# Performance work log

Hardware: AMD Instinct MI355X
Metric: run time of the kernel (lower is better)

The kernel has to match this reference:

```python
import jax, jax.numpy as jnp
import numpy as np

N = 20000      # nodes
E = 200000     # edges
F_IN = 512     # num_features
H = 1024       # hidden (hard-coded in module)
OUT = 128      # output_size


def setup_inputs() -> dict:
    key = jax.random.key(0)
    ks = jax.random.split(key, 12)
    x = jax.random.normal(ks[0], (N, F_IN), jnp.float32)
    edge_index = jax.random.randint(ks[1], (2, E), 0, N, dtype=jnp.int32)
    edge_weight = jax.random.uniform(ks[2], (E,), jnp.float32)
    # GCNConv weights (glorot-ish) and biases
    w1 = jax.random.normal(ks[3], (F_IN, H), jnp.float32) / np.sqrt(F_IN)
    b1 = jnp.zeros((H,), jnp.float32)
    w2 = jax.random.normal(ks[4], (H, OUT), jnp.float32) / np.sqrt(H)
    b2 = jnp.zeros((OUT,), jnp.float32)
    # residual Linear layers
    rw1 = jax.random.normal(ks[5], (F_IN, H), jnp.float32) / np.sqrt(F_IN)
    rb1 = jax.random.normal(ks[6], (H,), jnp.float32) * 0.01
    rw2 = jax.random.normal(ks[7], (H, OUT), jnp.float32) / np.sqrt(H)
    rb2 = jax.random.normal(ks[8], (OUT,), jnp.float32) * 0.01
    return {"x": x, "w1": w1, "b1": b1, "w2": w2, "b2": b2,
            "rw1": rw1, "rb1": rb1, "rw2": rw2, "rb2": rb2,
            "edge_weight": edge_weight, "edge_index": edge_index}


def gcn_conv(x, W, b, edge_index, edge_weight, n):
    """PyG GCNConv: linear transform, add self-loops (weight 1), sym-normalized scatter-add."""
    xw = x @ W                                             # [n, d_out]
    loop = jnp.arange(n, dtype=edge_index.dtype)
    row = jnp.concatenate([edge_index[0], loop])           # sources (x_j)
    col = jnp.concatenate([edge_index[1], loop])           # targets (aggregate here)
    ew = jnp.concatenate([edge_weight, jnp.ones((n,), xw.dtype)])
    deg = jax.ops.segment_sum(ew, col, num_segments=n)     # weighted in-degree
    dis = jnp.where(deg > 0, jax.lax.rsqrt(jnp.where(deg > 0, deg, 1.0)), 0.0)
    norm = dis[row] * ew * dis[col]                        # [E+n]
    msg = xw[row] * norm[:, None]                          # gather + scale
    out = jax.ops.segment_sum(msg, col, num_segments=n)    # scatter-add
    return out + b


def reference(x, w1, b1, w2, b2, rw1, rb1, rw2, rb2, edge_weight, edge_index):
    n = x.shape[0]
    h = jax.nn.relu(gcn_conv(x, w1, b1, edge_index, edge_weight, n) + (x @ rw1 + rb1))
    # F.dropout(training=False) is identity in eval mode
    out = gcn_conv(h, w2, b2, edge_index, edge_weight, n) + (h @ rw2 + rb2)
    return out
```

## Files before the change

kernel.cpp:

```cpp
#include <hip/hip_runtime.h>
#include <hip/hip_bf16.h>

#define NN 20000
#define EE 200000
#define FIN 512
#define HID 1024
#define OUTF 128
#define MPAD 20096

typedef unsigned short ush;
typedef __attribute__((ext_vector_type(8))) short bf16x8;
typedef __attribute__((ext_vector_type(4))) float f32x4;

__device__ __forceinline__ ush f2bf_rne(float f) {
    union { float f; unsigned u; } a; a.f = f;
    unsigned u = a.u;
    return (ush)((u + 0x7fffu + ((u >> 16) & 1u)) >> 16);
}
__device__ __forceinline__ float bf2f(ush h) {
    union { float f; unsigned u; } a; a.u = ((unsigned)h) << 16;
    return a.f;
}
__device__ __forceinline__ void split_bf(float v, ush& hi, ush& lo) {
    hi = f2bf_rne(v);
    lo = f2bf_rne(v - bf2f(hi));
}

__device__ __forceinline__ void gl16(const void* g, void* l) {
    __builtin_amdgcn_global_load_lds(
        (const __attribute__((address_space(1))) unsigned*)g,
        (__attribute__((address_space(3))) unsigned*)l, 16, 0, 0);
}

__global__ void init_kernel(float* deg, int* cnt, int n) {
    int i = blockIdx.x * blockDim.x + threadIdx.x;
    if (i < n) { deg[i] = 1.0f; cnt[i] = 0; }
}

__global__ void deg_count_kernel(const int* __restrict__ ei, const float* __restrict__ ew,
                                 float* deg, int* cnt, int e) {
    int idx = blockIdx.x * blockDim.x + threadIdx.x;
    if (idx < e) {
        int c = ei[EE + idx];
        atomicAdd(&deg[c], ew[idx]);
        atomicAdd(&cnt[c], 1);
    }
}

__global__ void dis_kernel(const float* __restrict__ deg, float* dis, int n) {
    int i = blockIdx.x * blockDim.x + threadIdx.x;
    if (i < n) dis[i] = rsqrtf(deg[i]);
}

__global__ void bias_kernel(const float* __restrict__ b1, const float* __restrict__ rb1,
                            const float* __restrict__ b2, const float* __restrict__ rb2,
                            float* bias1s, float* bias2c) {
    int i = blockIdx.x * blockDim.x + threadIdx.x;
    if (i < HID) bias1s[i] = b1[i] + rb1[i];
    if (i < 256) bias2c[i] = (i < 128) ? 0.0f : (b2[i - 128] + rb2[i - 128]);
}

#define SCAN_THREADS 1024
#define SCAN_CHUNK 20
__global__ __launch_bounds__(SCAN_THREADS)
void scan_kernel(const int* __restrict__ cnt, int* rowptr, int* cursor, int n, int total_e) {
    __shared__ int part[SCAN_THREADS];
    int t = threadIdx.x;
    int base = t * SCAN_CHUNK;
    int s = 0;
    for (int j = 0; j < SCAN_CHUNK; ++j) { int i = base + j; if (i < n) s += cnt[i]; }
    part[t] = s;
    __syncthreads();
    for (int off = 1; off < SCAN_THREADS; off <<= 1) {
        int add = (t >= off) ? part[t - off] : 0;
        __syncthreads();
        part[t] += add;
        __syncthreads();
    }
    int run = (t == 0) ? 0 : part[t - 1];
    for (int j = 0; j < SCAN_CHUNK; ++j) {
        int i = base + j;
        if (i < n) { rowptr[i] = run; cursor[i] = run; run += cnt[i]; }
    }
    if (t == SCAN_THREADS - 1) rowptr[n] = total_e;
}

__global__ void scatter_kernel(const int* __restrict__ ei, const float* __restrict__ ew,
                               const float* __restrict__ dis, int* cursor,
                               int* srcs, float* norms, int e) {
    int idx = blockIdx.x * blockDim.x + threadIdx.x;
    if (idx < e) {
        int r = ei[idx];
        int c = ei[EE + idx];
        float nv = dis[r] * ew[idx] * dis[c];
        int p = atomicAdd(&cursor[c], 1);
        srcs[p] = r;
        norms[p] = nv;
    }
}

__global__ __launch_bounds__(256)
void tsplit_kernel(const float* __restrict__ src, int K, int N,
                   ush* __restrict__ dh, ush* __restrict__ dl, int ldst, int koff) {
    __shared__ float tile[32][33];
    int tx = threadIdx.x & 31, ty = threadIdx.x >> 5;
    int n0 = blockIdx.x * 32, k0 = blockIdx.y * 32;
#pragma unroll
    for (int i = 0; i < 4; ++i)
        tile[ty * 4 + i][tx] = src[(size_t)(k0 + ty * 4 + i) * N + n0 + tx];
    __syncthreads();
#pragma unroll
    for (int i = 0; i < 4; ++i) {
        int n = n0 + ty * 4 + i, k = k0 + tx;
        float v = tile[tx][ty * 4 + i];
        ush h, lo; split_bf(v, h, lo);
        size_t off = (size_t)n * ldst + koff + k;
        dh[off] = h;
        dl[off] = lo;
    }
}

__global__ __launch_bounds__(128)
void aggx_kernel(const float* __restrict__ x,
                 ush* __restrict__ xh, ush* __restrict__ xl,
                 ush* __restrict__ axh, ush* __restrict__ axl,
                 const float* __restrict__ dis,
                 const int* __restrict__ rowptr, const int* __restrict__ srcs,
                 const float* __restrict__ norms) {
    int i = blockIdx.x;
    int t = threadIdx.x;
    float d = dis[i];
    float d2 = d * d;
    float4 v = ((const float4*)(x + (size_t)i * FIN))[t];

    ushort4 vh, vl;
    split_bf(v.x, vh.x, vl.x); split_bf(v.y, vh.y, vl.y);
    split_bf(v.z, vh.z, vl.z); split_bf(v.w, vh.w, vl.w);
    ((ushort4*)(xh + (size_t)i * FIN))[t] = vh;
    ((ushort4*)(xl + (size_t)i * FIN))[t] = vl;

    float s0 = d2 * v.x, s1 = d2 * v.y, s2 = d2 * v.z, s3 = d2 * v.w;
    int beg = rowptr[i], end = rowptr[i + 1];
    int j = beg;
    for (; j + 2 <= end; j += 2) {
        int sa = srcs[j], sb = srcs[j + 1];
        float wa = norms[j], wb = norms[j + 1];
        float4 ua = ((const float4*)(x + (size_t)sa * FIN))[t];
        float4 ub = ((const float4*)(x + (size_t)sb * FIN))[t];
        s0 += wa * ua.x + wb * ub.x;
        s1 += wa * ua.y + wb * ub.y;
        s2 += wa * ua.z + wb * ub.z;
        s3 += wa * ua.w + wb * ub.w;
    }
    if (j < end) {
        int sa = srcs[j];
        float wa = norms[j];
        float4 ua = ((const float4*)(x + (size_t)sa * FIN))[t];
        s0 += wa * ua.x; s1 += wa * ua.y; s2 += wa * ua.z; s3 += wa * ua.w;
    }
    ushort4 hv, lv;
    split_bf(s0, hv.x, lv.x); split_bf(s1, hv.y, lv.y);
    split_bf(s2, hv.z, lv.z); split_bf(s3, hv.w, lv.w);
    ((ushort4*)(axh + (size_t)i * FIN))[t] = hv;
    ((ushort4*)(axl + (size_t)i * FIN))[t] = lv;
}

__global__ __launch_bounds__(256)
void gemm_mfma(const ush* __restrict__ A0h, const ush* __restrict__ A0l,
               const ush* __restrict__ A1h, const ush* __restrict__ A1l,
               int ksw, int KA,
               const ush* __restrict__ BTh, const ush* __restrict__ BTl,
               const float* __restrict__ bias,
               float* __restrict__ Cf, ush* __restrict__ Chh, ush* __restrict__ Chl,
               int M, int N, int K, int mode) {
    __shared__ ush Ah[2][128 * 32], Al[2][128 * 32], Bh[2][128 * 32], Bl[2][128 * 32];

    int nwg = gridDim.x * gridDim.y;
    int orig = blockIdx.y * gridDim.x + blockIdx.x;
    int xcd = orig & 7, slot = orig >> 3;
    int q = nwg >> 3, r = nwg & 7;
    int wg = (xcd < r ? xcd * (q + 1) : r * (q + 1) + (xcd - r) * q) + slot;
    int bn = (wg % gridDim.x) * 128;
    int bm = (wg / gridDim.x) * 128;

    int t = threadIdx.x;
    int l = t & 63, w = t >> 6;
    int wr = w >> 1, wc = w & 1;

    int sr = t >> 2;
    int sg8 = (t & 3) * 8;
    size_t a_off0 = (size_t)(bm + sr) * KA + sg8;
    size_t a_off1 = (size_t)(bm + 64 + sr) * KA + sg8;
    size_t b_off0 = (size_t)(bn + sr) * K + sg8;
    size_t b_off1 = (size_t)(bn + 64 + sr) * K + sg8;
    int lo0 = t * 16, lo1 = t * 16 + 4096;

    int abase = (wr * 64 + (l & 15)) * 64 + ((l >> 4) << 4);
    int bbase = (wc * 64 + (l & 15)) * 64 + ((l >> 4) << 4);

    auto stage = [&](int kt, int b) {
        const ush* Asrch; const ush* Asrcl; int kk;
        if (kt < ksw) { Asrch = A0h; Asrcl = A0l; kk = kt; }
        else          { Asrch = A1h; Asrcl = A1l; kk = kt - ksw; }
        gl16(Asrch + a_off0 + kk, (char*)Ah[b] + lo0);
        gl16(Asrch + a_off1 + kk, (char*)Ah[b] + lo1);
        gl16(Asrcl + a_off0 + kk, (char*)Al[b] + lo0);
        gl16(Asrcl + a_off1 + kk, (char*)Al[b] + lo1);
        gl16(BTh + b_off0 + kt, (char*)Bh[b] + lo0);
        gl16(BTh + b_off1 + kt, (char*)Bh[b] + lo1);
        gl16(BTl + b_off0 + kt, (char*)Bl[b] + lo0);
        gl16(BTl + b_off1 + kt, (char*)Bl[b] + lo1);
    };

    f32x4 acc[4][4];
#pragma unroll
    for (int i = 0; i < 4; ++i)
#pragma unroll
        for (int j = 0; j < 4; ++j) acc[i][j] = (f32x4){0.f, 0.f, 0.f, 0.f};

    stage(0, 0);
    __syncthreads();

    int cur = 0;
    for (int kt = 0; kt < K; kt += 32) {
        if (kt + 32 < K) stage(kt + 32, cur ^ 1);

        bf16x8 ah[4], al[4], bh[4], bl[4];
#pragma unroll
        for (int f = 0; f < 4; ++f) {
            ah[f] = *(const bf16x8*)((const char*)Ah[cur] + abase + f * 1024);
            al[f] = *(const bf16x8*)((const char*)Al[cur] + abase + f * 1024);
            bh[f] = *(const bf16x8*)((const char*)Bh[cur] + bbase + f * 1024);
            bl[f] = *(const bf16x8*)((const char*)Bl[cur] + bbase + f * 1024);
        }
#pragma unroll
        for (int fm = 0; fm < 4; ++fm)
#pragma unroll
            for (int fn = 0; fn < 4; ++fn)
                acc[fm][fn] = __builtin_amdgcn_mfma_f32_16x16x32_bf16(ah[fm], bh[fn], acc[fm][fn], 0, 0, 0);
#pragma unroll
        for (int fm = 0; fm < 4; ++fm)
#pragma unroll
            for (int fn = 0; fn < 4; ++fn)
                acc[fm][fn] = __builtin_amdgcn_mfma_f32_16x16x32_bf16(ah[fm], bl[fn], acc[fm][fn], 0, 0, 0);
#pragma unroll
        for (int fm = 0; fm < 4; ++fm)
#pragma unroll
            for (int fn = 0; fn < 4; ++fn)
                acc[fm][fn] = __builtin_amdgcn_mfma_f32_16x16x32_bf16(al[fm], bh[fn], acc[fm][fn], 0, 0, 0);

        __syncthreads();
        cur ^= 1;
    }

    int ccol = bn + wc * 64 + (l & 15);
    float bb[4];
#pragma unroll
    for (int fn = 0; fn < 4; ++fn) bb[fn] = bias ? bias[ccol + fn * 16] : 0.0f;

    if (mode) {
#pragma unroll
        for (int fm = 0; fm < 4; ++fm)
#pragma unroll
            for (int j = 0; j < 4; ++j) {
                int row = bm + wr * 64 + fm * 16 + ((l >> 4) << 2) + j;
                if (row < M) {
#pragma unroll
                    for (int fn = 0; fn < 4; ++fn) {
                        float v = fmaxf(acc[fm][fn][j] + bb[fn], 0.0f);
                        ush hi, lo; split_bf(v, hi, lo);
                        size_t off = (size_t)row * N + ccol + fn * 16;
                        Chh[off] = hi;
                        Chl[off] = lo;
                    }
                }
            }
    } else {
#pragma unroll
        for (int fm = 0; fm < 4; ++fm)
#pragma unroll
            for (int j = 0; j < 4; ++j) {
                int row = bm + wr * 64 + fm * 16 + ((l >> 4) << 2) + j;
                if (row < M) {
#pragma unroll
                    for (int fn = 0; fn < 4; ++fn)
                        Cf[(size_t)row * N + ccol + fn * 16] = acc[fm][fn][j] + bb[fn];
                }
            }
    }
}

__global__ __launch_bounds__(256)
void agg2_kernel(const float* __restrict__ z2, const float* __restrict__ dis,
                 const int* __restrict__ rowptr, const int* __restrict__ srcs,
                 const float* __restrict__ norms, float* __restrict__ out) {
    int wave = threadIdx.x >> 6;
    int lane = threadIdx.x & 63;
    int i = blockIdx.x * 4 + wave;
    float d = dis[i];
    float d2 = d * d;
    float2 v = ((const float2*)(z2 + (size_t)i * 256))[lane];
    float ax = d2 * v.x, ay = d2 * v.y;
    int beg = rowptr[i], end = rowptr[i + 1];
    int j = beg;
    for (; j + 2 <= end; j += 2) {
        int sa = srcs[j], sb = srcs[j + 1];
        float wa = norms[j], wb = norms[j + 1];
        float2 ua = ((const float2*)(z2 + (size_t)sa * 256))[lane];
        float2 ub = ((const float2*)(z2 + (size_t)sb * 256))[lane];
        ax += wa * ua.x + wb * ub.x;
        ay += wa * ua.y + wb * ub.y;
    }
    if (j < end) {
        int sa = srcs[j];
        float wa = norms[j];
        float2 ua = ((const float2*)(z2 + (size_t)sa * 256))[lane];
        ax += wa * ua.x; ay += wa * ua.y;
    }
    float2 r = ((const float2*)(z2 + (size_t)i * 256 + 128))[lane];
    float2 o; o.x = ax + r.x; o.y = ay + r.y;
    ((float2*)(out + (size_t)i * OUTF))[lane] = o;
}

extern "C" void kernel_launch(void* const* d_in, const int* in_sizes, int n_in,
                              void* d_out, int out_size, void* d_ws, size_t ws_size,
                              hipStream_t stream) {
    const float* x   = (const float*)d_in[0];
    const float* w1  = (const float*)d_in[1];
    const float* b1  = (const float*)d_in[2];
    const float* w2  = (const float*)d_in[3];
    const float* b2  = (const float*)d_in[4];
    const float* rw1 = (const float*)d_in[5];
    const float* rb1 = (const float*)d_in[6];
    const float* rw2 = (const float*)d_in[7];
    const float* rb2 = (const float*)d_in[8];
    const float* ew  = (const float*)d_in[9];
    const int*   ei  = (const int*)d_in[10];
    float* out = (float*)d_out;

    char* p = (char*)d_ws;
    ush* xh  = (ush*)p; p += (size_t)MPAD * FIN * 2;
    ush* xl  = (ush*)p; p += (size_t)MPAD * FIN * 2;
    ush* axh = (ush*)p; p += (size_t)MPAD * FIN * 2;
    ush* axl = (ush*)p; p += (size_t)MPAD * FIN * 2;
    ush* hh  = (ush*)p; p += (size_t)MPAD * HID * 2;
    ush* hl  = (ush*)p; p += (size_t)MPAD * HID * 2;
    ush* w1cth = (ush*)p; p += (size_t)HID * HID * 2;
    ush* w1ctl = (ush*)p; p += (size_t)HID * HID * 2;
    ush* w2cth = (ush*)p; p += (size_t)256 * HID * 2;
    ush* w2ctl = (ush*)p; p += (size_t)256 * HID * 2;
    float* deg    = (float*)p; p += NN * 4;
    float* dis    = (float*)p; p += NN * 4;
    float* norms  = (float*)p; p += EE * 4;
    float* bias1s = (float*)p; p += HID * 4;
    float* bias2c = (float*)p; p += 256 * 4;
    int* rowptr = (int*)p; p += (NN + 1) * 4;
    int* cursor = (int*)p; p += NN * 4;
    int* cnt    = (int*)p; p += NN * 4;
    int* srcs   = (int*)p; p += EE * 4;
    float* z2 = (float*)xh;

    init_kernel<<<(NN + 255) / 256, 256, 0, stream>>>(deg, cnt, NN);
    deg_count_kernel<<<(EE + 255) / 256, 256, 0, stream>>>(ei, ew, deg, cnt, EE);
    dis_kernel<<<(NN + 255) / 256, 256, 0, stream>>>(deg, dis, NN);
    bias_kernel<<<(HID + 255) / 256, 256, 0, stream>>>(b1, rb1, b2, rb2, bias1s, bias2c);
    scan_kernel<<<1, SCAN_THREADS, 0, stream>>>(cnt, rowptr, cursor, NN, EE);
    scatter_kernel<<<(EE + 255) / 256, 256, 0, stream>>>(ei, ew, dis, cursor, srcs, norms, EE);

    { dim3 g(HID / 32, FIN / 32); tsplit_kernel<<<g, 256, 0, stream>>>(w1,  FIN, HID, w1cth, w1ctl, HID, 0);   }
    { dim3 g(HID / 32, FIN / 32); tsplit_kernel<<<g, 256, 0, stream>>>(rw1, FIN, HID, w1cth, w1ctl, HID, FIN); }
    { dim3 g(OUTF / 32, HID / 32); tsplit_kernel<<<g, 256, 0, stream>>>(w2,  HID, OUTF, w2cth, w2ctl, HID, 0); }
    { dim3 g(OUTF / 32, HID / 32); tsplit_kernel<<<g, 256, 0, stream>>>(rw2, HID, OUTF,
                                        w2cth + (size_t)128 * HID, w2ctl + (size_t)128 * HID, HID, 0); }

    aggx_kernel<<<NN, 128, 0, stream>>>(x, xh, xl, axh, axl, dis, rowptr, srcs, norms);

    {
        dim3 grid(HID / 128, MPAD / 128);
        gemm_mfma<<<grid, 256, 0, stream>>>(axh, axl, xh, xl, FIN, FIN,
                                            w1cth, w1ctl, bias1s,
                                            nullptr, hh, hl,
                                            NN, HID, HID, 1);
    }
    {
        dim3 grid(256 / 128, MPAD / 128);
        gemm_mfma<<<grid, 256, 0, stream>>>(hh, hl, hh, hl, HID, HID,
                                            w2cth, w2ctl, bias2c,
                                            z2, nullptr, nullptr,
                                            NN, 256, HID, 0);
    }
    agg2_kernel<<<NN / 4, 256, 0, stream>>>(z2, dis, rowptr, srcs, norms, out);
}
```

Measured before the change: 465.2 us.

## Replace first-layer GEMM with 256x256-tile, 4-stage pipelined MFMA kernel

Adds a dedicated kernel for the first-layer GEMM (aggregated x and x concatenated against the combined w1/rw1 weights, using a bf16 hi/lo split). It uses 256x256 output tiles with 512 threads and a 4-deep shared-memory ring of async global-to-LDS loads. The aim is more operand reuse per tile and better overlap of loads with MFMA work than the generic 128x128 double-buffered kernel. MPAD is enlarged to a multiple of 256 so the larger tiles cover all rows. In exchange the kernel holds 128 accumulator registers per thread and launches far fewer workgroups, which can lower occupancy and load balance across CUs.

```diff
diff --git a/kernel.cpp b/kernel.cpp
--- a/kernel.cpp
+++ b/kernel.cpp
@@ -6,7 +6,7 @@
 #define FIN 512
 #define HID 1024
 #define OUTF 128
-#define MPAD 20096
+#define MPAD 20224
 
 typedef unsigned short ush;
 typedef __attribute__((ext_vector_type(8))) short bf16x8;
@@ -163,6 +163,114 @@
     split_bf(s2, hv.z, lv.z); split_bf(s3, hv.w, lv.w);
     ((ushort4*)(axh + (size_t)i * FIN))[t] = hv;
     ((ushort4*)(axl + (size_t)i * FIN))[t] = lv;
+}
+
+__global__ __launch_bounds__(512, 2)
+void gemm256(const ush* __restrict__ axh, const ush* __restrict__ axl,
+             const ush* __restrict__ xh,  const ush* __restrict__ xl,
+             const ush* __restrict__ bth, const ush* __restrict__ btl,
+             const float* __restrict__ bias,
+             ush* __restrict__ Chh, ush* __restrict__ Chl) {
+    __shared__ ush LA[4 * 8192];
+    __shared__ ush LB[4 * 8192];
+
+    int nwg = gridDim.x * gridDim.y;
+    int orig = blockIdx.y * gridDim.x + blockIdx.x;
+    int xcd = orig & 7, slot0 = orig >> 3;
+    int q = nwg >> 3, r = nwg & 7;
+    int wg = (xcd < r ? xcd * (q + 1) : r * (q + 1) + (xcd - r) * q) + slot0;
+    int bn = (wg & 3) * 256;
+    int bm = (wg >> 2) * 256;
+
+    int t = threadIdx.x;
+    int l = t & 63, w = t >> 6;
+    int wr = w >> 2, wc = w & 3;
+
+    int cidx0 = t, cidx1 = t + 512;
+    int srow0 = cidx0 >> 2, srow1 = cidx1 >> 2;
+    int sc0 = (cidx0 & 3) ^ ((cidx0 >> 3) & 3);
+    int sc1 = (cidx1 & 3) ^ ((cidx1 >> 3) & 3);
+    int ld0 = cidx0 * 16, ld1 = cidx1 * 16;
+
+    int ksw16 = (((l >> 4) ^ ((l >> 1) & 3)) << 4);
+    int arow = wr * 128 + (l & 15);
+    int bcol = wc * 64 + (l & 15);
+
+    f32x4 acc[8][4];
+#pragma unroll
+    for (int i = 0; i < 8; ++i)
+#pragma unroll
+        for (int j = 0; j < 4; ++j) acc[i][j] = (f32x4){0.f, 0.f, 0.f, 0.f};
+
+    auto stage = [&](int kt, int s) {
+        int seg = kt >> 5;
+        int kk = (kt & 31) << 5;
+        const ush* Ap = (seg < 2) ? ((kk < FIN) ? axh : xh)
+                                  : ((kk < FIN) ? axl : xl);
+        int ka = kk & (FIN - 1);
+        const ush* Bp = (seg == 1) ? btl : bth;
+        char* la = (char*)LA + s * 16384;
+        char* lb = (char*)LB + s * 16384;
+        gl16(Ap + (size_t)(bm + srow0) * FIN + ka + sc0 * 8, la + ld0);
+        gl16(Ap + (size_t)(bm + srow1) * FIN + ka + sc1 * 8, la + ld1);
+        gl16(Bp + (size_t)(bn + srow0) * HID + kk + sc0 * 8, lb + ld0);
+        gl16(Bp + (size_t)(bn + srow1) * HID + kk + sc1 * 8, lb + ld1);
+    };
+
+    stage(0, 0); stage(1, 1); stage(2, 2);
+    asm volatile("s_waitcnt vmcnt(8)" ::: "memory");
+    __builtin_amdgcn_s_barrier();
+    __builtin_amdgcn_sched_barrier(0);
+
+    for (int kt = 0; kt < 96; ++kt) {
+        int s = kt & 3;
+        const char* la = (const char*)LA + s * 16384;
+        const char* lb = (const char*)LB + s * 16384;
+        bf16x8 a[8], b[4];
+#pragma unroll
+        for (int fm = 0; fm < 8; ++fm)
+            a[fm] = *(const bf16x8*)(la + (arow + fm * 16) * 64 + ksw16);
+#pragma unroll
+        for (int fn = 0; fn < 4; ++fn)
+            b[fn] = *(const bf16x8*)(lb + (bcol + fn * 16) * 64 + ksw16);
+
+        int nx = kt + 3; if (nx > 95) nx = 95;
+        stage(nx, (kt + 3) & 3);
+
+        __builtin_amdgcn_s_setprio(1);
+#pragma unroll
+        for (int fm = 0; fm < 8; ++fm)
+#pragma unroll
+            for (int fn = 0; fn < 4; ++fn)
+                acc[fm][fn] = __builtin_amdgcn_mfma_f32_16x16x32_bf16(a[fm], b[fn], acc[fm][fn], 0, 0, 0);
+        __builtin_amdgcn_s_setprio(0);
+
+        __builtin_amdgcn_sched_barrier(0);
+        asm volatile("s_waitcnt vmcnt(8)" ::: "memory");
+        __builtin_amdgcn_s_barrier();
+        __builtin_amdgcn_sched_barrier(0);
+    }
+
+    int ccol = bn + wc * 64 + (l & 15);
+    float bb[4];
+#pragma unroll
+    for (int fn = 0; fn < 4; ++fn) bb[fn] = bias[ccol + fn * 16];
+#pragma unroll
+    for (int fm = 0; fm < 8; ++fm)
+#pragma unroll
+        for (int j = 0; j < 4; ++j) {
+            int row = bm + wr * 128 + fm * 16 + ((l >> 4) << 2) + j;
+            if (row < NN) {
+#pragma unroll
+                for (int fn = 0; fn < 4; ++fn) {
+                    float v = fmaxf(acc[fm][fn][j] + bb[fn], 0.0f);
+                    ush hi, lo; split_bf(v, hi, lo);
+                    size_t off = (size_t)row * HID + ccol + fn * 16;
+                    Chh[off] = hi;
+                    Chl[off] = lo;
+                }
+            }
+        }
 }
 
 __global__ __launch_bounds__(256)
@@ -317,8 +425,8 @@
         float2 ua = ((const float2*)(z2 + (size_t)sa * 256))[lane];
         ax += wa * ua.x; ay += wa * ua.y;
     }
-    float2 r = ((const float2*)(z2 + (size_t)i * 256 + 128))[lane];
-    float2 o; o.x = ax + r.x; o.y = ay + r.y;
+    float2 rr = ((const float2*)(z2 + (size_t)i * 256 + 128))[lane];
+    float2 o; o.x = ax + rr.x; o.y = ay + rr.y;
     ((float2*)(out + (size_t)i * OUTF))[lane] = o;
 }
 
@@ -376,11 +484,8 @@
     aggx_kernel<<<NN, 128, 0, stream>>>(x, xh, xl, axh, axl, dis, rowptr, srcs, norms);
 
     {
-        dim3 grid(HID / 128, MPAD / 128);
-        gemm_mfma<<<grid, 256, 0, stream>>>(axh, axl, xh, xl, FIN, FIN,
-                                            w1cth, w1ctl, bias1s,
-                                            nullptr, hh, hl,
-                                            NN, HID, HID, 1);
+        dim3 grid(HID / 256, MPAD / 256);
+        gemm256<<<grid, 512, 0, stream>>>(axh, axl, xh, xl, w1cth, w1ctl, bias1s, hh, hl);
     }
     {
         dim3 grid(256 / 128, MPAD / 128);
```

Result: slower. 617.9 us (+32.8%).
